# Kernel tuning notes

Measured on AMD Instinct MI355X. Metric: run time of the kernel, lower is better.

The kernel has to match this reference:

```python
import jax, jax.numpy as jnp
import numpy as np
from jax import lax

IN_CH, HID, OUT_CH, N_MID, BATCH = 16, 8, 4, 60, 4194304


def setup_inputs() -> dict:
    key = jax.random.key(0)
    ks = jax.random.split(key, 7)
    scale = 1.0 / jnp.sqrt(jnp.float32(HID))  # keep 62-layer linear chain numerically stable
    x = jax.random.normal(ks[0], (BATCH, IN_CH), dtype=jnp.float32)
    W1 = jax.random.normal(ks[1], (HID, IN_CH), dtype=jnp.float32) * scale
    b1 = jax.random.normal(ks[2], (HID,), dtype=jnp.float32) * 0.01
    Ws = jax.random.normal(ks[3], (N_MID, HID, HID), dtype=jnp.float32) * scale
    bs = jax.random.normal(ks[4], (N_MID, HID), dtype=jnp.float32) * 0.01
    W2 = jax.random.normal(ks[5], (OUT_CH, HID), dtype=jnp.float32) * scale
    b2 = jax.random.normal(ks[6], (OUT_CH,), dtype=jnp.float32) * 0.01
    return {"x": x, "W1": W1, "b1": b1, "Ws": Ws, "bs": bs, "W2": W2, "b2": b2}


def reference(x, W1, b1, Ws, bs, W2, b2):
    # fc1: [B,16] -> [B,8]  (torch Linear: x @ W.T + b)
    h = x @ W1.T + b1

    # 60 sequential 8x8 Linear layers, no activation; scan over layer axis
    def step(h, wb):
        w, b = wb
        return h @ w.T + b, None

    h, _ = lax.scan(step, h, (Ws, bs))

    # fc2: [B,8] -> [B,4]
    return h @ W2.T + b2
```

## Files before the change

### kernel.cpp

```cpp
#include <hip/hip_runtime.h>

#define IN_CH  16
#define HID    8
#define OUT_CH 4
#define N_MID  60
#define BATCH  4194304

typedef float vfloat4 __attribute__((ext_vector_type(4)));

__global__ __launch_bounds__(64) void fold_kernel(
    const float* __restrict__ W1, const float* __restrict__ b1,
    const float* __restrict__ Ws, const float* __restrict__ bs,
    const float* __restrict__ W2, const float* __restrict__ b2,
    float* __restrict__ Mc ) {

    __shared__ float sWs[N_MID * HID * HID];
    __shared__ float sbs[N_MID * HID];
    __shared__ float A[2][HID][IN_CH];
    __shared__ float d[2][HID];

    const int t   = threadIdx.x;
    const int col = t & 15;
    const int r0  = t >> 4;

    {
        const float4* __restrict__ Ws4 = (const float4*)Ws;
        float4*       sW4              = (float4*)sWs;
        #pragma unroll
        for (int j = 0; j < (N_MID * HID * HID / 4) / 64; ++j)
            sW4[t + j * 64] = Ws4[t + j * 64];

        const float4* __restrict__ bs4 = (const float4*)bs;
        float4*       sb4              = (float4*)sbs;
        sb4[t] = bs4[t];
        if (t < (N_MID * HID / 4) - 64) sb4[t + 64] = bs4[t + 64];
    }

    if (t < (HID * IN_CH / 4)) ((float4*)&A[0][0][0])[t] = ((const float4*)W1)[t];
    if (t < HID) d[0][t] = b1[t];
    __syncthreads();

    int cur = 0;
    for (int l = 0; l < N_MID; ++l) {
        const float* W = sWs + l * HID * HID;
        float a0 = 0.f, a1 = 0.f;
        #pragma unroll
        for (int k = 0; k < HID; ++k) {
            const float av = A[cur][k][col];
            a0 += W[r0 * HID + k]       * av;
            a1 += W[(r0 + 4) * HID + k] * av;
        }
        float bc = 0.f;
        if (t < HID) {
            bc = sbs[l * HID + t];
            #pragma unroll
            for (int k = 0; k < HID; ++k)
                bc += W[t * HID + k] * d[cur][k];
        }
        A[1 - cur][r0][col]     = a0;
        A[1 - cur][r0 + 4][col] = a1;
        if (t < HID) d[1 - cur][t] = bc;
        cur ^= 1;
        __syncthreads();
    }

    {
        const int rr = t >> 4, cc = t & 15;
        float acc = 0.f;
        #pragma unroll
        for (int k = 0; k < HID; ++k)
            acc += W2[rr * HID + k] * A[cur][k][cc];
        Mc[rr * IN_CH + cc] = acc;
    }
    if (t < OUT_CH) {
        float acc = b2[t];
        #pragma unroll
        for (int k = 0; k < HID; ++k)
            acc += W2[t * HID + k] * d[cur][k];
        Mc[OUT_CH * IN_CH + t] = acc;
    }
}

#define ITERS 8

__global__ __launch_bounds__(256) void apply_kernel(
    const float* __restrict__ x,
    const float* __restrict__ Mc,
    float* __restrict__ out) {

    const int tid = threadIdx.x;
    const int q   = tid & 3;

    const float4* M4 = (const float4*)Mc;
    const float4 m0 = M4[0 * 4 + q];
    const float4 m1 = M4[1 * 4 + q];
    const float4 m2 = M4[2 * 4 + q];
    const float4 m3 = M4[3 * 4 + q];
    const float  cb = Mc[OUT_CH * IN_CH + q];

    const vfloat4* __restrict__ x4 = (const vfloat4*)x;
    const size_t g0     = (size_t)blockIdx.x * 256 + tid;
    const size_t stride = (size_t)gridDim.x * 256;

    vfloat4 xv[ITERS];
    #pragma unroll
    for (int j = 0; j < ITERS; ++j)
        xv[j] = __builtin_nontemporal_load(&x4[g0 + j * stride]);

    const bool hi2 = (q & 2) != 0;
    const bool lo1 = (q & 1) != 0;

    #pragma unroll
    for (int j = 0; j < ITERS; ++j) {
        const vfloat4 v = xv[j];
        float p0 = m0.x * v.x + m0.y * v.y + m0.z * v.z + m0.w * v.w;
        float p1 = m1.x * v.x + m1.y * v.y + m1.z * v.z + m1.w * v.w;
        float p2 = m2.x * v.x + m2.y * v.y + m2.z * v.z + m2.w * v.w;
        float p3 = m3.x * v.x + m3.y * v.y + m3.z * v.z + m3.w * v.w;

        float send_a = hi2 ? p0 : p2;
        float send_b = hi2 ? p1 : p3;
        float recv_a = __shfl_xor(send_a, 2);
        float recv_b = __shfl_xor(send_b, 2);
        float k0 = (hi2 ? p2 : p0) + recv_a;
        float k1 = (hi2 ? p3 : p1) + recv_b;
        float send = lo1 ? k0 : k1;
        float recv = __shfl_xor(send, 1);
        float val  = (lo1 ? k1 : k0) + recv + cb;

        __builtin_nontemporal_store(val, &out[g0 + j * stride]);
    }
}

extern "C" void kernel_launch(void* const* d_in, const int* in_sizes, int n_in,
                              void* d_out, int out_size, void* d_ws, size_t ws_size,
                              hipStream_t stream) {
    const float* x  = (const float*)d_in[0];
    const float* W1 = (const float*)d_in[1];
    const float* b1 = (const float*)d_in[2];
    const float* Ws = (const float*)d_in[3];
    const float* bs = (const float*)d_in[4];
    const float* W2 = (const float*)d_in[5];
    const float* b2 = (const float*)d_in[6];
    float* out = (float*)d_out;
    float* Mc  = (float*)d_ws;

    fold_kernel<<<1, 64, 0, stream>>>(W1, b1, Ws, bs, W2, b2, Mc);

    const int blocks = (BATCH * (IN_CH / 4)) / (256 * ITERS);
    apply_kernel<<<blocks, 256, 0, stream>>>(x, Mc, out);
}
```

Before: 388.0 us.

## Split 60-layer weight fold across four waves and combine partial products

The weight-folding kernel now runs with 256 threads. Each of four wavefronts composes 15 of the 60 hidden layers in registers, exchanging matrix entries with wave shuffles instead of shared memory and a barrier per layer. The four partial affine maps are then combined with three small 8x8 matrix products in shared memory before fc2 is folded in. This shortens the serial dependency chain of the single-block prologue and removes most of its barriers, at the cost of extra combine steps and slightly different floating-point association.

```diff
diff --git a/kernel.cpp b/kernel.cpp
--- a/kernel.cpp
+++ b/kernel.cpp
@@ -8,7 +8,7 @@
 
 typedef float vfloat4 __attribute__((ext_vector_type(4)));
 
-__global__ __launch_bounds__(64) void fold_kernel(
+__global__ __launch_bounds__(256) void fold_kernel(
     const float* __restrict__ W1, const float* __restrict__ b1,
     const float* __restrict__ Ws, const float* __restrict__ bs,
     const float* __restrict__ W2, const float* __restrict__ b2,
@@ -16,67 +16,121 @@
 
     __shared__ float sWs[N_MID * HID * HID];
     __shared__ float sbs[N_MID * HID];
-    __shared__ float A[2][HID][IN_CH];
-    __shared__ float d[2][HID];
+    __shared__ float sW2[OUT_CH * HID];
+    __shared__ float sb2[OUT_CH];
+    __shared__ float pA[4][HID][IN_CH];
+    __shared__ float pv[4][HID];
+    __shared__ float cA[2][HID][IN_CH];
+    __shared__ float cv[2][HID];
 
     const int t   = threadIdx.x;
-    const int col = t & 15;
-    const int r0  = t >> 4;
+    const int w   = t >> 6;
+    const int lid = t & 63;
+    const int col = lid & 15;
+    const int r0  = lid >> 4;
 
     {
         const float4* __restrict__ Ws4 = (const float4*)Ws;
         float4*       sW4              = (float4*)sWs;
         #pragma unroll
-        for (int j = 0; j < (N_MID * HID * HID / 4) / 64; ++j)
-            sW4[t + j * 64] = Ws4[t + j * 64];
+        for (int j = 0; j < 3; ++j)
+            sW4[t + j * 256] = Ws4[t + j * 256];
+        if (t < 960 - 768) sW4[t + 768] = Ws4[t + 768];
 
         const float4* __restrict__ bs4 = (const float4*)bs;
         float4*       sb4              = (float4*)sbs;
-        sb4[t] = bs4[t];
-        if (t < (N_MID * HID / 4) - 64) sb4[t + 64] = bs4[t + 64];
-    }
-
-    if (t < (HID * IN_CH / 4)) ((float4*)&A[0][0][0])[t] = ((const float4*)W1)[t];
-    if (t < HID) d[0][t] = b1[t];
+        if (t < (N_MID * HID / 4)) sb4[t] = bs4[t];
+
+        if (t < OUT_CH * HID) sW2[t] = W2[t];
+        if (t < OUT_CH)       sb2[t] = b2[t];
+    }
+
+    float a0, a1, dv0, dv1;
+    if (w == 0) {
+        a0  = W1[r0 * IN_CH + col];
+        a1  = W1[(r0 + 4) * IN_CH + col];
+        dv0 = b1[r0];
+        dv1 = b1[r0 + 4];
+    } else {
+        a0  = (col == r0)     ? 1.f : 0.f;
+        a1  = (col == r0 + 4) ? 1.f : 0.f;
+        dv0 = 0.f;
+        dv1 = 0.f;
+    }
     __syncthreads();
 
-    int cur = 0;
-    for (int l = 0; l < N_MID; ++l) {
-        const float* W = sWs + l * HID * HID;
-        float a0 = 0.f, a1 = 0.f;
-        #pragma unroll
-        for (int k = 0; k < HID; ++k) {
-            const float av = A[cur][k][col];
-            a0 += W[r0 * HID + k]       * av;
-            a1 += W[(r0 + 4) * HID + k] * av;
+    const int base = w * 15;
+    #pragma unroll
+    for (int l = 0; l < 15; ++l) {
+        const float* Wl = sWs + (base + l) * HID * HID;
+        const float4 wA = *(const float4*)(Wl + r0 * HID);
+        const float4 wB = *(const float4*)(Wl + r0 * HID + 4);
+        const float4 wC = *(const float4*)(Wl + (r0 + 4) * HID);
+        const float4 wD = *(const float4*)(Wl + (r0 + 4) * HID + 4);
+        const float w0[8] = {wA.x, wA.y, wA.z, wA.w, wB.x, wB.y, wB.z, wB.w};
+        const float w4[8] = {wC.x, wC.y, wC.z, wC.w, wD.x, wD.y, wD.z, wD.w};
+
+        float na0 = 0.f, na1 = 0.f;
+        float nd0 = sbs[(base + l) * HID + r0];
+        float nd1 = sbs[(base + l) * HID + r0 + 4];
+        #pragma unroll
+        for (int k = 0; k < 8; ++k) {
+            const int src = ((k & 3) << 4) | col;
+            const float Ak = __shfl((k < 4) ? a0 : a1, src);
+            const float dk = __shfl((k < 4) ? dv0 : dv1, src);
+            na0 += w0[k] * Ak;
+            na1 += w4[k] * Ak;
+            nd0 += w0[k] * dk;
+            nd1 += w4[k] * dk;
         }
-        float bc = 0.f;
-        if (t < HID) {
-            bc = sbs[l * HID + t];
+        a0 = na0; a1 = na1; dv0 = nd0; dv1 = nd1;
+    }
+
+    pA[w][r0][col]     = a0;
+    pA[w][r0 + 4][col] = a1;
+    if (col == 0) { pv[w][r0] = dv0; pv[w][r0 + 4] = dv1; }
+
+    if (t < HID * IN_CH) cA[0][t >> 4][t & 15] = 0.f;
+    __syncthreads();
+    if (t < HID * IN_CH) cA[0][t >> 4][t & 15] = pA[0][t >> 4][t & 15];
+    if (t < HID)         cv[0][t] = pv[0][t];
+    __syncthreads();
+
+    int cb = 0;
+    #pragma unroll
+    for (int s = 1; s < 4; ++s) {
+        if (t < HID * IN_CH) {
+            const int r = t >> 4, c = t & 15;
+            float acc = 0.f;
             #pragma unroll
             for (int k = 0; k < HID; ++k)
-                bc += W[t * HID + k] * d[cur][k];
+                acc += pA[s][r][k] * cA[cb][k][c];
+            cA[1 - cb][r][c] = acc;
         }
-        A[1 - cur][r0][col]     = a0;
-        A[1 - cur][r0 + 4][col] = a1;
-        if (t < HID) d[1 - cur][t] = bc;
-        cur ^= 1;
+        if (t < HID) {
+            float acc = pv[s][t];
+            #pragma unroll
+            for (int k = 0; k < HID; ++k)
+                acc += pA[s][t][k] * cv[cb][k];
+            cv[1 - cb][t] = acc;
+        }
+        cb ^= 1;
         __syncthreads();
     }
 
-    {
-        const int rr = t >> 4, cc = t & 15;
+    if (t < OUT_CH * IN_CH) {
+        const int r = t >> 4, c = t & 15;
         float acc = 0.f;
         #pragma unroll
         for (int k = 0; k < HID; ++k)
-            acc += W2[rr * HID + k] * A[cur][k][cc];
-        Mc[rr * IN_CH + cc] = acc;
+            acc += sW2[r * HID + k] * cA[cb][k][c];
+        Mc[r * IN_CH + c] = acc;
     }
     if (t < OUT_CH) {
-        float acc = b2[t];
+        float acc = sb2[t];
         #pragma unroll
         for (int k = 0; k < HID; ++k)
-            acc += W2[t * HID + k] * d[cur][k];
+            acc += sW2[t * HID + k] * cv[cb][k];
         Mc[OUT_CH * IN_CH + t] = acc;
     }
 }
@@ -145,7 +199,7 @@
     float* out = (float*)d_out;
     float* Mc  = (float*)d_ws;
 
-    fold_kernel<<<1, 64, 0, stream>>>(W1, b1, Ws, bs, W2, b2, Mc);
+    fold_kernel<<<1, 256, 0, stream>>>(W1, b1, Ws, bs, W2, b2, Mc);
 
     const int blocks = (BATCH * (IN_CH / 4)) / (256 * ITERS);
     apply_kernel<<<blocks, 256, 0, stream>>>(x, Mc, out);
```

After: 380.5 us. About the same (-1.9%).
